# Optimization experiments

Measured on AMD Instinct MI355X. Metric: run time of the kernel, lower is better.

Reference implementation:

```python
import jax, jax.numpy as jnp
import numpy as np

D_MODEL = 1024
N_HEADS = 16
D_HEAD = D_MODEL // N_HEADS
D_FF = 4096
B, T = 2, 2048


def setup_inputs() -> dict:
    key = jax.random.key(0)
    ks = jax.random.split(key, 8)
    s = 0.02
    return {
        "x": jax.random.normal(ks[0], (B, T, D_MODEL), dtype=jnp.float32),
        "wq": jax.random.normal(ks[1], (D_MODEL, D_MODEL), dtype=jnp.float32) * s,
        "wk": jax.random.normal(ks[2], (D_MODEL, D_MODEL), dtype=jnp.float32) * s,
        "wv": jax.random.normal(ks[3], (D_MODEL, D_MODEL), dtype=jnp.float32) * s,
        "wo": jax.random.normal(ks[4], (D_MODEL, D_MODEL), dtype=jnp.float32) * s,
        "w1": jax.random.normal(ks[5], (D_FF, D_MODEL), dtype=jnp.float32) * s,
        "b1": jnp.zeros((D_FF,), dtype=jnp.float32),
        "w2": jax.random.normal(ks[6], (D_MODEL, D_FF), dtype=jnp.float32) * s,
        "b2": jnp.zeros((D_MODEL,), dtype=jnp.float32),
        "ln1_g": jnp.ones((D_MODEL,), dtype=jnp.float32),
        "ln1_b": jnp.zeros((D_MODEL,), dtype=jnp.float32),
        "ln2_g": jnp.ones((D_MODEL,), dtype=jnp.float32),
        "ln2_b": jnp.zeros((D_MODEL,), dtype=jnp.float32),
    }


def _layernorm(x, g, b, eps=1e-5):
    mu = jnp.mean(x, axis=-1, keepdims=True)
    var = jnp.mean(jnp.square(x - mu), axis=-1, keepdims=True)
    return (x - mu) * jax.lax.rsqrt(var + eps) * g + b


def reference(x, wq, wk, wv, wo, w1, b1, w2, b2, ln1_g, ln1_b, ln2_g, ln2_b):
    Bsz, Tlen, C = x.shape
    h = _layernorm(x, ln1_g, ln1_b)
    # torch Linear: y = h @ W^T ; reshape to [B, H, T, Dh]
    def proj(w):
        return (h @ w.T).reshape(Bsz, Tlen, N_HEADS, D_HEAD).transpose(0, 2, 1, 3)
    q, k, v = proj(wq), proj(wk), proj(wv)
    scores = jnp.einsum('bhqd,bhkd->bhqk', q, k) / np.sqrt(D_HEAD).astype(np.float32)
    p = jax.nn.softmax(scores.astype(jnp.float32), axis=-1).astype(scores.dtype)
    out = jnp.einsum('bhqk,bhkd->bhqd', p, v)
    out = out.transpose(0, 2, 1, 3).reshape(Bsz, Tlen, C)
    x = x + out @ wo.T
    h2 = _layernorm(x, ln2_g, ln2_b)
    ff = jax.nn.gelu(h2 @ w1.T + b1, approximate=False) @ w2.T + b2
    return x + ff
```

## Files before the change

kernel.cpp:

```cpp
#include <hip/hip_runtime.h>
#include <hip/hip_bf16.h>
#include <math.h>

#define DM   1024
#define NH   16
#define DH   64
#define DFF  4096
#define BB   2
#define TT   2048
#define MTOK (BB*TT)
#define QS   3072

typedef unsigned short u16;
typedef unsigned int   u32;
typedef __attribute__((ext_vector_type(8))) __bf16 bf16x8;
typedef __attribute__((ext_vector_type(4))) float  f32x4;

__device__ inline float bf2f(u16 u) { return __uint_as_float(((u32)u) << 16); }
__device__ inline u16 f2bf(float f) {
  u32 u = __float_as_uint(f);
  u += 0x7FFFu + ((u >> 16) & 1u);
  return (u16)(u >> 16);
}
__device__ inline u32 packtrunc(float lo, float hi) {
  return __builtin_amdgcn_perm(__float_as_uint(hi), __float_as_uint(lo), 0x07060302u);
}
__device__ inline float fexp2(float x) { return __builtin_amdgcn_exp2f(x); }

__device__ inline void gload_lds16(const void* g, void* l) {
  __builtin_amdgcn_global_load_lds(
      (const __attribute__((address_space(1))) void*)g,
      (__attribute__((address_space(3))) void*)l,
      16, 0, 0);
}

__global__ __launch_bounds__(256) void prep(
    const float* __restrict__ wq, const float* __restrict__ wk, const float* __restrict__ wv,
    const float* __restrict__ wo, const float* __restrict__ w1, const float* __restrict__ w2,
    const float* __restrict__ x, const float* __restrict__ g, const float* __restrict__ be,
    u16* __restrict__ wqkv_b, u16* __restrict__ wo_b, u16* __restrict__ w1_b,
    u16* __restrict__ w2_b, u16* __restrict__ h1)
{
  const int blk = blockIdx.x;
  if (blk < 12288) {
    const float* src; u16* dst; int idx;
    if (blk < 3072) {
      idx = blk * 256 + threadIdx.x;
      const int sel = idx >> 18;
      const int j = idx & 0x3FFFF;
      src = sel == 0 ? wq : (sel == 1 ? wk : wv);
      dst = wqkv_b;
      float4 v = ((const float4*)src)[j];
      ushort4 o; o.x = f2bf(v.x); o.y = f2bf(v.y); o.z = f2bf(v.z); o.w = f2bf(v.w);
      ((ushort4*)dst)[idx] = o;
      return;
    } else if (blk < 4096) { src = wo; dst = wo_b; idx = (blk - 3072) * 256 + threadIdx.x; }
    else if (blk < 8192)   { src = w1; dst = w1_b; idx = (blk - 4096) * 256 + threadIdx.x; }
    else                   { src = w2; dst = w2_b; idx = (blk - 8192) * 256 + threadIdx.x; }
    float4 v = ((const float4*)src)[idx];
    ushort4 o; o.x = f2bf(v.x); o.y = f2bf(v.y); o.z = f2bf(v.z); o.w = f2bf(v.w);
    ((ushort4*)dst)[idx] = o;
    return;
  }
  const int w = threadIdx.x >> 6, lane = threadIdx.x & 63;
  const int row = (blk - 12288) * 4 + w;
  const float4* xr = (const float4*)(x + (size_t)row * DM);
  float4 v[4];
  float s = 0.f, s2 = 0.f;
#pragma unroll
  for (int i = 0; i < 4; i++) {
    v[i] = xr[i * 64 + lane];
    s  += v[i].x + v[i].y + v[i].z + v[i].w;
    s2 += v[i].x * v[i].x + v[i].y * v[i].y + v[i].z * v[i].z + v[i].w * v[i].w;
  }
#pragma unroll
  for (int off = 32; off > 0; off >>= 1) {
    s  += __shfl_xor(s,  off);
    s2 += __shfl_xor(s2, off);
  }
  const float mu = s * (1.f / DM);
  const float rs = rsqrtf(s2 * (1.f / DM) - mu * mu + 1e-5f);
  u16* orow = h1 + (size_t)row * DM;
#pragma unroll
  for (int i = 0; i < 4; i++) {
    const float4 gg = ((const float4*)g)[i * 64 + lane];
    const float4 bb = ((const float4*)be)[i * 64 + lane];
    ushort4 o;
    o.x = f2bf((v[i].x - mu) * rs * gg.x + bb.x);
    o.y = f2bf((v[i].y - mu) * rs * gg.y + bb.y);
    o.z = f2bf((v[i].z - mu) * rs * gg.z + bb.z);
    o.w = f2bf((v[i].w - mu) * rs * gg.w + bb.w);
    ((ushort4*)orow)[i * 64 + lane] = o;
  }
}

__global__ __launch_bounds__(256) void reduce_ln(
    const float* __restrict__ x, const float* __restrict__ P,
    const float* __restrict__ g, const float* __restrict__ be,
    float* __restrict__ xmid, u16* __restrict__ h2)
{
  const float* P0 = P;
  const float* P1 = P + (size_t)MTOK * DM;
  const int w = threadIdx.x >> 6, lane = threadIdx.x & 63;
  const int row = blockIdx.x * 4 + w;
  const size_t roff = (size_t)row * DM;
  float4 v[4];
  float s = 0.f, s2 = 0.f;
#pragma unroll
  for (int i = 0; i < 4; i++) {
    const float4 a = ((const float4*)(x  + roff))[i * 64 + lane];
    const float4 p = ((const float4*)(P0 + roff))[i * 64 + lane];
    const float4 qv = ((const float4*)(P1 + roff))[i * 64 + lane];
    v[i].x = a.x + p.x + qv.x; v[i].y = a.y + p.y + qv.y;
    v[i].z = a.z + p.z + qv.z; v[i].w = a.w + p.w + qv.w;
    ((float4*)(xmid + roff))[i * 64 + lane] = v[i];
    s  += v[i].x + v[i].y + v[i].z + v[i].w;
    s2 += v[i].x * v[i].x + v[i].y * v[i].y + v[i].z * v[i].z + v[i].w * v[i].w;
  }
#pragma unroll
  for (int off = 32; off > 0; off >>= 1) {
    s  += __shfl_xor(s,  off);
    s2 += __shfl_xor(s2, off);
  }
  const float mu = s * (1.f / DM);
  const float rs = rsqrtf(s2 * (1.f / DM) - mu * mu + 1e-5f);
  u16* orow = h2 + roff;
#pragma unroll
  for (int i = 0; i < 4; i++) {
    const float4 gg = ((const float4*)g)[i * 64 + lane];
    const float4 bb = ((const float4*)be)[i * 64 + lane];
    ushort4 o;
    o.x = f2bf((v[i].x - mu) * rs * gg.x + bb.x);
    o.y = f2bf((v[i].y - mu) * rs * gg.y + bb.y);
    o.z = f2bf((v[i].z - mu) * rs * gg.z + bb.z);
    o.w = f2bf((v[i].w - mu) * rs * gg.w + bb.w);
    ((ushort4*)orow)[i * 64 + lane] = o;
  }
}

__global__ __launch_bounds__(256) void reduce_out(
    const float* __restrict__ Q, const float* __restrict__ xmid,
    const float* __restrict__ b2, float* __restrict__ out)
{
  const float* Q0 = Q;
  const float* Q1 = Q + (size_t)MTOK * DM;
  const int i = blockIdx.x * 256 + threadIdx.x;
  const float4 a = ((const float4*)xmid)[i];
  const float4 p = ((const float4*)Q0)[i];
  const float4 qv = ((const float4*)Q1)[i];
  const float4 bb = ((const float4*)b2)[i & (DM / 4 - 1)];
  float4 o;
  o.x = a.x + p.x + qv.x + bb.x; o.y = a.y + p.y + qv.y + bb.y;
  o.z = a.z + p.z + qv.z + bb.z; o.w = a.w + p.w + qv.w + bb.w;
  ((float4*)out)[i] = o;
}

template <int EPI, int BN>
__global__ __launch_bounds__(256) void gemm_bt(
    const u16* __restrict__ A, const u16* __restrict__ Bw,
    int M, int N, int K,
    const float* __restrict__ bias,
    u16* __restrict__ outB, float oscale, int scaleN)
{
  constexpr int NJ = BN / 32;
  __shared__ u16 As[128 * 64];
  __shared__ u16 Bs[BN * 64];

  const int tid  = threadIdx.x;
  const int w    = tid >> 6;
  const int lane = tid & 63;
  const int wr   = w >> 1, wc = w & 1;
  const int q    = lane >> 4;
  const int li   = lane & 15;
  const int rowBase = blockIdx.y * 128;
  const int colBase = blockIdx.x * BN;

  const int lr = lane >> 3;
  const int cs = (lane & 7) ^ lr;
  const u16* Abase = A  + (size_t)(rowBase + lr) * K + cs * 8;
  const u16* Bbase = Bw + (size_t)(colBase + lr) * K + cs * 8;

  f32x4 acc[4][NJ] = {};

  for (int k0 = 0; k0 < K; k0 += 64) {
    __syncthreads();
#pragma unroll
    for (int jj = 0; jj < 4; jj++) {
      const int rb = (w * 4 + jj) * 8;
      gload_lds16(Abase + (size_t)rb * K + k0, &As[rb * 64]);
    }
#pragma unroll
    for (int jj = 0; jj < NJ; jj++) {
      const int rb = (w * NJ + jj) * 8;
      gload_lds16(Bbase + (size_t)rb * K + k0, &Bs[rb * 64]);
    }
    __syncthreads();
#pragma unroll
    for (int kk = 0; kk < 2; kk++) {
      bf16x8 fa[4], fb[NJ];
      const int pos = (kk * 4 + q) ^ (li & 7);
#pragma unroll
      for (int i = 0; i < 4; i++) {
        const int row = wr * 64 + i * 16 + li;
        fa[i] = *(const bf16x8*)&As[row * 64 + pos * 8];
      }
#pragma unroll
      for (int j = 0; j < NJ; j++) {
        const int row = wc * (BN / 2) + j * 16 + li;
        fb[j] = *(const bf16x8*)&Bs[row * 64 + pos * 8];
      }
#pragma unroll
      for (int i = 0; i < 4; i++)
#pragma unroll
        for (int j = 0; j < NJ; j++)
          acc[i][j] = __builtin_amdgcn_mfma_f32_16x16x32_bf16(fa[i], fb[j], acc[i][j], 0, 0, 0);
    }
  }

#pragma unroll
  for (int i = 0; i < 4; i++) {
#pragma unroll
    for (int j = 0; j < NJ; j++) {
      const int col = colBase + wc * (BN / 2) + j * 16 + li;
      float bv = 0.f;
      if constexpr (EPI == 2) bv = bias[col];
#pragma unroll
      for (int r = 0; r < 4; r++) {
        const int row = rowBase + wr * 64 + i * 16 + q * 4 + r;
        float v = acc[i][j][r] + bv;
        if constexpr (EPI == 2) {
          const float z = fexp2(-v * (2.302213f + 0.1029625f * v * v));
          v = v * __builtin_amdgcn_rcpf(1.f + z);
        }
        if constexpr (EPI == 0) {
          const float sc = (col < scaleN) ? oscale : 1.f;
          v *= sc;
        }
        outB[(size_t)row * N + col] = f2bf(v);
      }
    }
  }
}

__global__ __launch_bounds__(256) void gemm_sk(
    const u16* __restrict__ A, const u16* __restrict__ Bw,
    int N, int K, int KLEN, float* __restrict__ P)
{
  __shared__ u16 As[128 * 64];
  __shared__ u16 Bs[64 * 64];

  const int tid  = threadIdx.x;
  const int w    = tid >> 6;
  const int lane = tid & 63;
  const int wr   = w >> 1, wc = w & 1;
  const int q    = lane >> 4;
  const int li   = lane & 15;
  const int rowBase = blockIdx.y * 128;
  const int colBase = blockIdx.x * 64;
  const int koff = blockIdx.z * KLEN;

  const int lr = lane >> 3;
  const int cs = (lane & 7) ^ lr;
  const u16* Abase = A  + (size_t)(rowBase + lr) * K + koff + cs * 8;
  const u16* Bbase = Bw + (size_t)(colBase + lr) * K + koff + cs * 8;

  f32x4 acc[4][2] = {};

  for (int k0 = 0; k0 < KLEN; k0 += 64) {
    __syncthreads();
#pragma unroll
    for (int jj = 0; jj < 4; jj++) {
      const int rb = (w * 4 + jj) * 8;
      gload_lds16(Abase + (size_t)rb * K + k0, &As[rb * 64]);
    }
#pragma unroll
    for (int jj = 0; jj < 2; jj++) {
      const int rb = (w * 2 + jj) * 8;
      gload_lds16(Bbase + (size_t)rb * K + k0, &Bs[rb * 64]);
    }
    __syncthreads();
#pragma unroll
    for (int kk = 0; kk < 2; kk++) {
      bf16x8 fa[4], fb[2];
      const int pos = (kk * 4 + q) ^ (li & 7);
#pragma unroll
      for (int i = 0; i < 4; i++) {
        const int row = wr * 64 + i * 16 + li;
        fa[i] = *(const bf16x8*)&As[row * 64 + pos * 8];
      }
#pragma unroll
      for (int j = 0; j < 2; j++) {
        const int row = wc * 32 + j * 16 + li;
        fb[j] = *(const bf16x8*)&Bs[row * 64 + pos * 8];
      }
#pragma unroll
      for (int i = 0; i < 4; i++)
#pragma unroll
        for (int j = 0; j < 2; j++)
          acc[i][j] = __builtin_amdgcn_mfma_f32_16x16x32_bf16(fa[i], fb[j], acc[i][j], 0, 0, 0);
    }
  }

  float* Pz = P + (size_t)blockIdx.z * MTOK * DM;
#pragma unroll
  for (int i = 0; i < 4; i++)
#pragma unroll
    for (int j = 0; j < 2; j++) {
      const int col = colBase + wc * 32 + j * 16 + li;
#pragma unroll
      for (int r = 0; r < 4; r++) {
        const int row = rowBase + wr * 64 + i * 16 + q * 4 + r;
        Pz[(size_t)row * N + col] = acc[i][j][r];
      }
    }
}

__global__ __launch_bounds__(256) void transpose_v(
    const u16* __restrict__ vq, u16* __restrict__ vt)
{
  __shared__ u16 t[64][72];
  const int bh = blockIdx.x, b = bh >> 4, h = bh & 15;
  const int t0 = blockIdx.y * 64;
  const int tid = threadIdx.x;
  const int r = tid >> 2, c = (tid & 3) * 16;
  const u16* src = vq + (size_t)(b * TT + t0 + r) * QS + h * DH + c;
#pragma unroll
  for (int i = 0; i < 4; i++)
    *(ushort4*)&t[r][c + i * 4] = ((const ushort4*)src)[i];
  __syncthreads();
  const int dh = tid >> 2, tt = (tid & 3) * 16;
  u16* dst = vt + ((size_t)bh * 64 + dh) * TT + t0 + tt;
#pragma unroll
  for (int i = 0; i < 4; i++) {
    ushort4 o;
    o.x = t[tt + i * 4 + 0][dh]; o.y = t[tt + i * 4 + 1][dh];
    o.z = t[tt + i * 4 + 2][dh]; o.w = t[tt + i * 4 + 3][dh];
    ((ushort4*)dst)[i] = o;
  }
}

__global__ __launch_bounds__(256) void attn_mfma(
    const u16* __restrict__ qb, const u16* __restrict__ kb,
    const u16* __restrict__ vt, u16* __restrict__ ob)
{
  __shared__ u16 Ks[2][64 * 64];
  __shared__ u16 Vs[2][64 * 64];
  __shared__ u16 Sh[4 * 32 * 72];

  const int tid = threadIdx.x, w = tid >> 6, lane = tid & 63;
  const int q = lane >> 4, li = lane & 15;
  const int bh = blockIdx.x, b = bh >> 4, h = bh & 15;
  const int q0 = blockIdx.y * 128;
  const int lr8 = lane >> 3, lc8 = lane & 7;

#pragma unroll
  for (int jj = 0; jj < 4; jj++) {
    const int rb = w * 32 + jj * 8;
    const int row = rb + lr8;
    const int cs = lc8 ^ (row & 7);
    gload_lds16(qb + (size_t)(b * TT + q0 + row) * QS + h * DH + cs * 8,
                &Sh[rb * 64]);
  }
  __syncthreads();

  bf16x8 qf[2][2];
#pragma unroll
  for (int n = 0; n < 2; n++)
#pragma unroll
    for (int kk = 0; kk < 2; kk++) {
      const int row = w * 32 + n * 16 + li;
      const int pos = (kk * 4 + q) ^ (li & 7);
      qf[n][kk] = *(const bf16x8*)&Sh[row * 64 + pos * 8];
    }

  auto stage = [&](int buf, int kt) {
#pragma unroll
    for (int half = 0; half < 2; half++) {
      const int rb = w * 16 + half * 8;
      const int row = rb + lr8;
      const int cs = lc8 ^ (row & 7);
      gload_lds16(kb + (size_t)(b * TT + kt + row) * QS + h * DH + cs * 8,
                  &Ks[buf][rb * 64]);
      gload_lds16(vt + ((size_t)bh * 64 + row) * TT + kt + cs * 8,
                  &Vs[buf][rb * 64]);
    }
  };

  f32x4 ot[4][2] = {};
  float lsum[2] = {0.f, 0.f};
  u16* Pw = &Sh[w * 32 * 72];

  stage(0, 0);
  for (int it = 0; it < TT / 64; it++) {
    __syncthreads();
    if (it + 1 < TT / 64) stage((it + 1) & 1, (it + 1) * 64);
    const u16* Kc = Ks[it & 1];
    const u16* Vc = Vs[it & 1];

    f32x4 st[4][2] = {};
#pragma unroll
    for (int kk = 0; kk < 2; kk++)
#pragma unroll
      for (int i = 0; i < 4; i++) {
        const int pos = (kk * 4 + q) ^ (li & 7);
        const bf16x8 kf = *(const bf16x8*)&Kc[(i * 16 + li) * 64 + pos * 8];
#pragma unroll
        for (int n = 0; n < 2; n++)
          st[i][n] = __builtin_amdgcn_mfma_f32_16x16x32_bf16(kf, qf[n][kk], st[i][n], 0, 0, 0);
      }

    u32 pk[4][2][2];
#pragma unroll
    for (int i = 0; i < 4; i++)
#pragma unroll
      for (int n = 0; n < 2; n++) {
        const float p0 = fexp2(st[i][n][0]);
        const float p1 = fexp2(st[i][n][1]);
        const float p2 = fexp2(st[i][n][2]);
        const float p3 = fexp2(st[i][n][3]);
        lsum[n] += (p0 + p1) + (p2 + p3);
        pk[i][n][0] = packtrunc(p0, p1);
        pk[i][n][1] = packtrunc(p2, p3);
      }

#pragma unroll
    for (int i = 0; i < 4; i++)
#pragma unroll
      for (int n = 0; n < 2; n++) {
        const int a = (n * 16 + li) * 72 + i * 16 + q * 4;
        *(u32*)&Pw[a]     = pk[i][n][0];
        *(u32*)&Pw[a + 2] = pk[i][n][1];
      }

#pragma unroll
    for (int kk = 0; kk < 2; kk++) {
      bf16x8 pf[2];
#pragma unroll
      for (int n = 0; n < 2; n++)
        pf[n] = *(const bf16x8*)&Pw[(n * 16 + li) * 72 + kk * 32 + q * 8];
#pragma unroll
      for (int m = 0; m < 4; m++) {
        const int pos = (kk * 4 + q) ^ (li & 7);
        const bf16x8 vf = *(const bf16x8*)&Vc[(m * 16 + li) * 64 + pos * 8];
#pragma unroll
        for (int n = 0; n < 2; n++)
          ot[m][n] = __builtin_amdgcn_mfma_f32_16x16x32_bf16(vf, pf[n], ot[m][n], 0, 0, 0);
      }
    }
  }

  float inv[2];
#pragma unroll
  for (int n = 0; n < 2; n++) {
    float s = lsum[n];
    s += __shfl_xor(s, 16);
    s += __shfl_xor(s, 32);
    inv[n] = 1.f / s;
  }
#pragma unroll
  for (int m = 0; m < 4; m++)
#pragma unroll
    for (int n = 0; n < 2; n++) {
      const int a = (n * 16 + li) * 72 + m * 16 + q * 4;
      *(u32*)&Pw[a]     = packtrunc(ot[m][n][0] * inv[n], ot[m][n][1] * inv[n]);
      *(u32*)&Pw[a + 2] = packtrunc(ot[m][n][2] * inv[n], ot[m][n][3] * inv[n]);
    }
#pragma unroll
  for (int pass = 0; pass < 4; pass++) {
    const int row = pass * 8 + lr8;
    const bf16x8 v = *(const bf16x8*)&Pw[row * 72 + lc8 * 8];
    const int token = q0 + w * 32 + row;
    *(bf16x8*)(ob + ((size_t)(b * TT + token) * NH + h) * DH + lc8 * 8) = v;
  }
}

extern "C" void kernel_launch(void* const* d_in, const int* in_sizes, int n_in,
                              void* d_out, int out_size, void* d_ws, size_t ws_size,
                              hipStream_t stream) {
  const float* x    = (const float*)d_in[0];
  const float* wq   = (const float*)d_in[1];
  const float* wk   = (const float*)d_in[2];
  const float* wv   = (const float*)d_in[3];
  const float* wo   = (const float*)d_in[4];
  const float* w1   = (const float*)d_in[5];
  const float* b1   = (const float*)d_in[6];
  const float* w2   = (const float*)d_in[7];
  const float* b2   = (const float*)d_in[8];
  const float* ln1g = (const float*)d_in[9];
  const float* ln1b = (const float*)d_in[10];
  const float* ln2g = (const float*)d_in[11];
  const float* ln2b = (const float*)d_in[12];

  size_t off = 0;
  char* base = (char*)d_ws;
  auto alloc = [&](size_t bytes) { void* p = base + off; off += bytes; return p; };

  u16* wqkv_b = (u16*)alloc((size_t)3 * DM * DM * 2);
  u16* wo_b   = (u16*)alloc((size_t)DM * DM * 2);
  u16* w1_b   = (u16*)alloc((size_t)DFF * DM * 2);
  u16* w2_b   = (u16*)alloc((size_t)DM * DFF * 2);
  u16* h1     = (u16*)alloc((size_t)MTOK * DM * 2);
  u16* qkvb   = (u16*)alloc((size_t)MTOK * QS * 2);
  u16* attn   = (u16*)alloc((size_t)MTOK * DM * 2);
  u16* h2     = (u16*)alloc((size_t)MTOK * DM * 2);
  u16* ff1    = (u16*)alloc((size_t)MTOK * DFF * 2);
  float* xmid = (float*)alloc((size_t)MTOK * DM * 4);
  u16* vtb    = ff1;
  float* woP  = (float*)ff1;
  float* ff2P = (float*)h1;
  (void)ws_size; (void)in_sizes; (void)n_in; (void)out_size;

  prep<<<13312, 256, 0, stream>>>(wq, wk, wv, wo, w1, w2, x, ln1g, ln1b,
                                  wqkv_b, wo_b, w1_b, w2_b, h1);

  const float QSCALE = 0.125f * 1.44269504088896340736f;
  gemm_bt<0, 128><<<dim3(QS / 128, MTOK / 128), 256, 0, stream>>>(
      h1, wqkv_b, MTOK, QS, DM, nullptr, qkvb, QSCALE, DM);

  transpose_v<<<dim3(BB * NH, TT / 64), 256, 0, stream>>>(qkvb + 2 * DM, vtb);
  attn_mfma<<<dim3(BB * NH, TT / 128), 256, 0, stream>>>(qkvb, qkvb + DM, vtb, attn);

  gemm_sk<<<dim3(DM / 64, MTOK / 128, 2), 256, 0, stream>>>(
      attn, wo_b, DM, DM, DM / 2, woP);
  reduce_ln<<<MTOK / 4, 256, 0, stream>>>(x, woP, ln2g, ln2b, xmid, h2);

  gemm_bt<2, 128><<<dim3(DFF / 128, MTOK / 128), 256, 0, stream>>>(
      h2, w1_b, MTOK, DFF, DM, b1, ff1, 1.f, 0);
  gemm_sk<<<dim3(DM / 64, MTOK / 128, 2), 256, 0, stream>>>(
      ff1, w2_b, DM, DFF, DFF / 2, ff2P);
  reduce_out<<<MTOK * DM / 4 / 256, 256, 0, stream>>>(ff2P, xmid, b2, (float*)d_out);
}
```

Baseline: 350.0 us.

## Use 8 waves of 16 query rows each in attention kernel

The attention kernel now launches 512 threads per block instead of 256. Each of the 8 waves owns 16 query rows instead of 32, so per-wave accumulators and Q fragments are halved, and each wave stages only one 8-row slice of K and V. The aim is more waves in flight per block to hide LDS and global latency and to lower register pressure. In exchange, each K/V fragment read from LDS feeds one MFMA instead of two, so LDS traffic per FLOP doubles, and there are more barriers per unit of work.

```diff
diff --git a/kernel.cpp b/kernel.cpp
--- a/kernel.cpp
+++ b/kernel.cpp
@@ -339,13 +339,13 @@
   }
 }
 
-__global__ __launch_bounds__(256) void attn_mfma(
+__global__ __launch_bounds__(512) void attn_mfma(
     const u16* __restrict__ qb, const u16* __restrict__ kb,
     const u16* __restrict__ vt, u16* __restrict__ ob)
 {
   __shared__ u16 Ks[2][64 * 64];
   __shared__ u16 Vs[2][64 * 64];
-  __shared__ u16 Sh[4 * 32 * 72];
+  __shared__ u16 Sh[8 * 16 * 72];
 
   const int tid = threadIdx.x, w = tid >> 6, lane = tid & 63;
   const int q = lane >> 4, li = lane & 15;
@@ -354,8 +354,8 @@
   const int lr8 = lane >> 3, lc8 = lane & 7;
 
 #pragma unroll
-  for (int jj = 0; jj < 4; jj++) {
-    const int rb = w * 32 + jj * 8;
+  for (int jj = 0; jj < 2; jj++) {
+    const int rb = w * 16 + jj * 8;
     const int row = rb + lr8;
     const int cs = lc8 ^ (row & 7);
     gload_lds16(qb + (size_t)(b * TT + q0 + row) * QS + h * DH + cs * 8,
@@ -363,32 +363,27 @@
   }
   __syncthreads();
 
-  bf16x8 qf[2][2];
-#pragma unroll
-  for (int n = 0; n < 2; n++)
-#pragma unroll
-    for (int kk = 0; kk < 2; kk++) {
-      const int row = w * 32 + n * 16 + li;
-      const int pos = (kk * 4 + q) ^ (li & 7);
-      qf[n][kk] = *(const bf16x8*)&Sh[row * 64 + pos * 8];
-    }
+  bf16x8 qf[2];
+#pragma unroll
+  for (int kk = 0; kk < 2; kk++) {
+    const int row = w * 16 + li;
+    const int pos = (kk * 4 + q) ^ (li & 7);
+    qf[kk] = *(const bf16x8*)&Sh[row * 64 + pos * 8];
+  }
 
   auto stage = [&](int buf, int kt) {
-#pragma unroll
-    for (int half = 0; half < 2; half++) {
-      const int rb = w * 16 + half * 8;
-      const int row = rb + lr8;
-      const int cs = lc8 ^ (row & 7);
-      gload_lds16(kb + (size_t)(b * TT + kt + row) * QS + h * DH + cs * 8,
-                  &Ks[buf][rb * 64]);
-      gload_lds16(vt + ((size_t)bh * 64 + row) * TT + kt + cs * 8,
-                  &Vs[buf][rb * 64]);
-    }
+    const int rb = w * 8;
+    const int row = rb + lr8;
+    const int cs = lc8 ^ (row & 7);
+    gload_lds16(kb + (size_t)(b * TT + kt + row) * QS + h * DH + cs * 8,
+                &Ks[buf][rb * 64]);
+    gload_lds16(vt + ((size_t)bh * 64 + row) * TT + kt + cs * 8,
+                &Vs[buf][rb * 64]);
   };
 
-  f32x4 ot[4][2] = {};
-  float lsum[2] = {0.f, 0.f};
-  u16* Pw = &Sh[w * 32 * 72];
+  f32x4 ot[4] = {};
+  float lsum = 0.f;
+  u16* Pw = &Sh[w * 16 * 72];
 
   stage(0, 0);
   for (int it = 0; it < TT / 64; it++) {
@@ -397,79 +392,62 @@
     const u16* Kc = Ks[it & 1];
     const u16* Vc = Vs[it & 1];
 
-    f32x4 st[4][2] = {};
+    f32x4 st[4] = {};
 #pragma unroll
     for (int kk = 0; kk < 2; kk++)
 #pragma unroll
       for (int i = 0; i < 4; i++) {
         const int pos = (kk * 4 + q) ^ (li & 7);
         const bf16x8 kf = *(const bf16x8*)&Kc[(i * 16 + li) * 64 + pos * 8];
-#pragma unroll
-        for (int n = 0; n < 2; n++)
-          st[i][n] = __builtin_amdgcn_mfma_f32_16x16x32_bf16(kf, qf[n][kk], st[i][n], 0, 0, 0);
-      }
-
-    u32 pk[4][2][2];
-#pragma unroll
-    for (int i = 0; i < 4; i++)
-#pragma unroll
-      for (int n = 0; n < 2; n++) {
-        const float p0 = fexp2(st[i][n][0]);
-        const float p1 = fexp2(st[i][n][1]);
-        const float p2 = fexp2(st[i][n][2]);
-        const float p3 = fexp2(st[i][n][3]);
-        lsum[n] += (p0 + p1) + (p2 + p3);
-        pk[i][n][0] = packtrunc(p0, p1);
-        pk[i][n][1] = packtrunc(p2, p3);
-      }
-
-#pragma unroll
-    for (int i = 0; i < 4; i++)
-#pragma unroll
-      for (int n = 0; n < 2; n++) {
-        const int a = (n * 16 + li) * 72 + i * 16 + q * 4;
-        *(u32*)&Pw[a]     = pk[i][n][0];
-        *(u32*)&Pw[a + 2] = pk[i][n][1];
-      }
+        st[i] = __builtin_amdgcn_mfma_f32_16x16x32_bf16(kf, qf[kk], st[i], 0, 0, 0);
+      }
+
+    u32 pk[4][2];
+#pragma unroll
+    for (int i = 0; i < 4; i++) {
+      const float p0 = fexp2(st[i][0]);
+      const float p1 = fexp2(st[i][1]);
+      const float p2 = fexp2(st[i][2]);
+      const float p3 = fexp2(st[i][3]);
+      lsum += (p0 + p1) + (p2 + p3);
+      pk[i][0] = packtrunc(p0, p1);
+      pk[i][1] = packtrunc(p2, p3);
+    }
+
+#pragma unroll
+    for (int i = 0; i < 4; i++) {
+      const int a = li * 72 + i * 16 + q * 4;
+      *(u32*)&Pw[a]     = pk[i][0];
+      *(u32*)&Pw[a + 2] = pk[i][1];
+    }
 
 #pragma unroll
     for (int kk = 0; kk < 2; kk++) {
-      bf16x8 pf[2];
-#pragma unroll
-      for (int n = 0; n < 2; n++)
-        pf[n] = *(const bf16x8*)&Pw[(n * 16 + li) * 72 + kk * 32 + q * 8];
+      const bf16x8 pf = *(const bf16x8*)&Pw[li * 72 + kk * 32 + q * 8];
 #pragma unroll
       for (int m = 0; m < 4; m++) {
         const int pos = (kk * 4 + q) ^ (li & 7);
         const bf16x8 vf = *(const bf16x8*)&Vc[(m * 16 + li) * 64 + pos * 8];
-#pragma unroll
-        for (int n = 0; n < 2; n++)
-          ot[m][n] = __builtin_amdgcn_mfma_f32_16x16x32_bf16(vf, pf[n], ot[m][n], 0, 0, 0);
-      }
-    }
-  }
-
-  float inv[2];
-#pragma unroll
-  for (int n = 0; n < 2; n++) {
-    float s = lsum[n];
-    s += __shfl_xor(s, 16);
-    s += __shfl_xor(s, 32);
-    inv[n] = 1.f / s;
-  }
-#pragma unroll
-  for (int m = 0; m < 4; m++)
-#pragma unroll
-    for (int n = 0; n < 2; n++) {
-      const int a = (n * 16 + li) * 72 + m * 16 + q * 4;
-      *(u32*)&Pw[a]     = packtrunc(ot[m][n][0] * inv[n], ot[m][n][1] * inv[n]);
-      *(u32*)&Pw[a + 2] = packtrunc(ot[m][n][2] * inv[n], ot[m][n][3] * inv[n]);
-    }
-#pragma unroll
-  for (int pass = 0; pass < 4; pass++) {
+        ot[m] = __builtin_amdgcn_mfma_f32_16x16x32_bf16(vf, pf, ot[m], 0, 0, 0);
+      }
+    }
+  }
+
+  float s = lsum;
+  s += __shfl_xor(s, 16);
+  s += __shfl_xor(s, 32);
+  const float inv = 1.f / s;
+#pragma unroll
+  for (int m = 0; m < 4; m++) {
+    const int a = li * 72 + m * 16 + q * 4;
+    *(u32*)&Pw[a]     = packtrunc(ot[m][0] * inv, ot[m][1] * inv);
+    *(u32*)&Pw[a + 2] = packtrunc(ot[m][2] * inv, ot[m][3] * inv);
+  }
+#pragma unroll
+  for (int pass = 0; pass < 2; pass++) {
     const int row = pass * 8 + lr8;
     const bf16x8 v = *(const bf16x8*)&Pw[row * 72 + lc8 * 8];
-    const int token = q0 + w * 32 + row;
+    const int token = q0 + w * 16 + row;
     *(bf16x8*)(ob + ((size_t)(b * TT + token) * NH + h) * DH + lc8 * 8) = v;
   }
 }
@@ -518,7 +496,7 @@
       h1, wqkv_b, MTOK, QS, DM, nullptr, qkvb, QSCALE, DM);
 
   transpose_v<<<dim3(BB * NH, TT / 64), 256, 0, stream>>>(qkvb + 2 * DM, vtb);
-  attn_mfma<<<dim3(BB * NH, TT / 128), 256, 0, stream>>>(qkvb, qkvb + DM, vtb, attn);
+  attn_mfma<<<dim3(BB * NH, TT / 128), 512, 0, stream>>>(qkvb, qkvb + DM, vtb, attn);
 
   gemm_sk<<<dim3(DM / 64, MTOK / 128, 2), 256, 0, stream>>>(
       attn, wo_b, DM, DM, DM / 2, woP);
```

Result: faster. 336.1 us (-4.0%).
